# Optimization experiments

Measured on AMD Instinct MI355X. Metric: run time of the kernel, lower is better.

Reference implementation:

```python
import jax, jax.numpy as jnp
import numpy as np

WS = 2
D = 128  # hidden_dim per direction
SCALE_X = float(np.sqrt(2.0))  # rescale=True, highway_bias=0 -> sqrt(1+exp(0))


def sru_bidir(x, W, wc, b, k):
    """Bidirectional single-layer SRU (sru lib, layer_norm=False, rescale=True).
    x: (L, N, din). Returns (L, N, 2*D)."""
    L, N, _ = x.shape
    U = (x @ W).reshape(L, N, 2, D, k)  # (L,N,dir,D,k)
    vf, vr = wc.reshape(2, 2, D)  # each (dir, D)
    bf, br = b.reshape(2, 2, D)
    # time-reverse the backward direction so one scan handles both
    U = jnp.concatenate([U[:, :, :1], U[::-1, :, 1:]], axis=2)
    if k == 4:
        xprime = U[..., 3]
    else:
        xp = x.reshape(L, N, 2, D)
        xprime = jnp.concatenate([xp[:, :, :1], xp[::-1, :, 1:]], axis=2) * SCALE_X

    def step(c, inp):
        u0, u1, u2, xpt = inp  # each (N,2,D)
        f = jax.nn.sigmoid(u1 + vf * c + bf)
        c = f * c + (1.0 - f) * u0
        r = jax.nn.sigmoid(u2 + vr * c + br)
        h = r * c + (1.0 - r) * xpt
        return c, h

    c0 = jnp.zeros((N, 2, D), dtype=x.dtype)
    _, H = jax.lax.scan(step, c0, (U[..., 0], U[..., 1], U[..., 2], xprime))
    # un-reverse backward direction outputs
    H = jnp.concatenate([H[:, :, :1], H[::-1, :, 1:]], axis=2)
    return H.reshape(L, N, 2 * D)


def setup_inputs() -> dict:
    key = jax.random.key(0)
    ks = jax.random.split(key, 6)
    B, C, Himg, Wimg = 8, 3, 224, 224
    F = WS * WS * C  # 12
    inp = {
        "x": jax.random.normal(ks[0], (B, C, Himg, Wimg), jnp.float32),
        "W1": jax.random.normal(ks[1], (F, 2 * D * 4), jnp.float32) * (1.0 / np.sqrt(F)),
        "wc1": jax.random.normal(ks[2], (2 * 2 * D,), jnp.float32) * 0.1,
        "b1": jnp.zeros((2 * 2 * D,), jnp.float32),
        "W2": jax.random.normal(ks[3], (2 * D, 2 * D * 3), jnp.float32) * (1.0 / np.sqrt(2 * D)),
        "wc2": jax.random.normal(ks[4], (2 * 2 * D,), jnp.float32) * 0.1,
        "b2": jnp.zeros((2 * 2 * D,), jnp.float32),
    }
    return inp


def reference(x, W1, wc1, b1, W2, wc2, b2):
    B, C, Himg, Wimg = x.shape
    Hp, Wp = Himg // WS, Wimg // WS
    F = WS * WS * C
    # get_valid_patches: (B, Hp, Wp, C*ws*ws) with (C, wh, ww) flatten order
    p = x.reshape(B, C, Hp, WS, Wp, WS).transpose(0, 2, 4, 1, 3, 5).reshape(B, Hp, Wp, F)
    # input_array = patches.permute(2,0,3,1) -> (Hp, B, Wp, F)
    # apply_one_direction on firstVRNN: merge Hp into batch, scan over Wp
    a1 = p.transpose(1, 0, 2, 3).reshape(Hp * B, Wp, F).transpose(1, 0, 2)  # (Wp, Hp*B, F)
    h1 = sru_bidir(a1, W1, wc1, b1, k=4)  # (Wp, Hp*B, 2D)
    h1 = h1.transpose(1, 0, 2).reshape(Hp, B, Wp, 2 * D)
    # vertical_results = out.permute(2,1,0,3) -> (Wp, B, Hp, 2D)
    v = h1.transpose(2, 1, 0, 3)
    # second direction: merge Wp into batch, scan over Hp
    a2 = v.reshape(Wp * B, Hp, 2 * D).transpose(1, 0, 2)  # (Hp, Wp*B, 2D)
    h2 = sru_bidir(a2, W2, wc2, b2, k=3)  # (Hp, Wp*B, 2D)
    h2 = h2.transpose(1, 0, 2).reshape(Wp, B, Hp, 2 * D)
    # feature_map.permute(1,3,2,0) -> (B, 2D, Hp, Wp)
    return h2.transpose(1, 3, 2, 0)
```

## Files before the change

kernel.cpp:

```cpp
#include <hip/hip_runtime.h>
#include <hip/hip_bf16.h>

typedef unsigned short ushort_t;
typedef unsigned int uint_t;

typedef __bf16 bf16x8 __attribute__((ext_vector_type(8)));
typedef float f32x4 __attribute__((ext_vector_type(4)));

__device__ __forceinline__ float bf2f(ushort_t u) {
    return __uint_as_float(((uint_t)u) << 16);
}
__device__ __forceinline__ ushort_t f2bf(float f) {
    uint_t x = __float_as_uint(f);
    uint_t r = (x + 0x7FFFu + ((x >> 16) & 1u)) >> 16;
    return (ushort_t)r;
}
__device__ __forceinline__ float sigmoidf_fast(float x) {
    return 1.0f / (1.0f + __expf(-x));
}

#define PP 12544
#define PLANE 25690112ULL

__global__ __launch_bounds__(256) void permute_w2(const float* __restrict__ W2,
                                                  ushort_t* __restrict__ W2t) {
    int i = blockIdx.x * 256 + threadIdx.x;
    int np = i >> 8;
    int k  = i & 255;
    int kk  = np >> 8;
    int rem = np & 255;
    int dir = rem >> 7;
    int d   = rem & 127;
    int oc = dir * 384 + d * 3 + kk;
    W2t[np * 256 + k] = f2bf(W2[k * 768 + oc]);
}

__global__ __launch_bounds__(256) void scan1(const float* __restrict__ x,
                                             const float* __restrict__ W1,
                                             const float* __restrict__ wc1,
                                             const float* __restrict__ b1,
                                             ushort_t* __restrict__ H1a,
                                             ushort_t* __restrict__ U2t) {
    __shared__ float patch[112 * 12];
    __shared__ ushort_t hbuf[112 * 258];
    const int n1 = blockIdx.x;
    const int hp = n1 >> 3, b = n1 & 7;
    const int tid = threadIdx.x;
    const float SCALE_X = 1.41421356237309515f;

    for (int e = tid; e < 1344; e += 256) {
        int c = e / 448;
        int rem = e % 448;
        int wh = rem / 224;
        int pos = rem % 224;
        float v = x[((b * 3 + c) * 224 + (2 * hp + wh)) * 224 + pos];
        patch[(pos >> 1) * 12 + c * 4 + wh * 2 + (pos & 1)] = v;
    }

    float4 w[12];
    const float4* W1v = (const float4*)W1;
#pragma unroll
    for (int j = 0; j < 12; ++j) w[j] = W1v[j * 256 + tid];

    const float vf = wc1[tid],       vr = wc1[256 + tid];
    const float bfv = b1[tid],       brv = b1[256 + tid];
    const int dir = tid >> 7;

    __syncthreads();

    float cst = 0.0f;
    for (int t = 0; t < 112; ++t) {
        const int tt = dir ? (111 - t) : t;
        const float4* pp = (const float4*)(patch + tt * 12);
        float4 p0 = pp[0], p1 = pp[1], p2 = pp[2];
        float pj[12] = {p0.x, p0.y, p0.z, p0.w, p1.x, p1.y, p1.z, p1.w,
                        p2.x, p2.y, p2.z, p2.w};
        float u0 = 0.f, u1 = 0.f, u2 = 0.f, u3 = 0.f;
#pragma unroll
        for (int j = 0; j < 12; ++j) {
            float pv = pj[j];
            u0 = fmaf(w[j].x, pv, u0);
            u1 = fmaf(w[j].y, pv, u1);
            u2 = fmaf(w[j].z, pv, u2);
            u3 = fmaf(w[j].w, pv, u3);
        }
        float f = sigmoidf_fast(u1 + vf * cst + bfv);
        cst = f * cst + (1.0f - f) * u0;
        float r = sigmoidf_fast(u2 + vr * cst + brv);
        float h = r * cst + (1.0f - r) * u3;
        H1a[((size_t)b * PP + hp * 112 + tt) * 256 + tid] = f2bf(h);
        hbuf[tt * 258 + tid] = f2bf(h * SCALE_X);
    }

    __syncthreads();
    const size_t base3 = 3 * PLANE + (size_t)b * 256 * PP + (size_t)hp * 112;
    for (int e = tid; e < 28672; e += 256) {
        int ch = e / 112;
        int wp = e - ch * 112;
        U2t[base3 + (size_t)ch * PP + wp] = hbuf[wp * 258 + ch];
    }
}

__global__ __launch_bounds__(256) void gemm2(const ushort_t* __restrict__ A,
                                             const ushort_t* __restrict__ Bt,
                                             ushort_t* __restrict__ U2t) {
    __shared__ ushort_t As[2][128 * 32];
    __shared__ ushort_t Bs[2][128 * 32];
    const int m0 = blockIdx.y * 128;
    const int bb = blockIdx.y / 98;
    const int p0 = (blockIdx.y % 98) * 128;
    const int n0 = blockIdx.x * 128;
    const int kidx = n0 >> 8;
    const int ch0  = n0 & 255;
    const int tid = threadIdx.x;
    const int w = tid >> 6, lane = tid & 63;
    const int wm = w >> 1, wn = w & 1;
    const int lr = lane >> 2;
    const int lc = (lane & 3) * 8;
    const int ln16 = lane & 15;
    const int k8 = (lane >> 4) * 8;

    f32x4 acc[4][4] = {};

    for (int kb = 0; kb < 256; kb += 64) {
        if (kb) __syncthreads();
#pragma unroll
        for (int h = 0; h < 2; ++h) {
#pragma unroll
            for (int q = 0; q < 2; ++q) {
                int r = w * 32 + q * 16;
                const ushort_t* gA = A + (size_t)(m0 + r + lr) * 256 + kb + h * 32 + lc;
                __builtin_amdgcn_global_load_lds(
                    (const __attribute__((address_space(1))) uint_t*)gA,
                    (__attribute__((address_space(3))) uint_t*)(As[h] + r * 32), 16, 0, 0);
                const ushort_t* gB = Bt + (size_t)(n0 + r + lr) * 256 + kb + h * 32 + lc;
                __builtin_amdgcn_global_load_lds(
                    (const __attribute__((address_space(1))) uint_t*)gB,
                    (__attribute__((address_space(3))) uint_t*)(Bs[h] + r * 32), 16, 0, 0);
            }
        }
        __syncthreads();

#pragma unroll
        for (int h = 0; h < 2; ++h) {
            bf16x8 af[4], bf[4];
#pragma unroll
            for (int i = 0; i < 4; ++i) {
                af[i] = *(const bf16x8*)(As[h] + (wm * 64 + i * 16 + ln16) * 32 + k8);
                bf[i] = *(const bf16x8*)(Bs[h] + (wn * 64 + i * 16 + ln16) * 32 + k8);
            }
#pragma unroll
            for (int i = 0; i < 4; ++i)
#pragma unroll
                for (int j = 0; j < 4; ++j)
                    acc[i][j] = __builtin_amdgcn_mfma_f32_16x16x32_bf16(
                        af[i], bf[j], acc[i][j], 0, 0, 0);
        }
    }

    const int rq = (lane >> 4) * 4;
    const size_t planeBase = (size_t)kidx * PLANE + (size_t)(bb * 256 + ch0) * PP;
#pragma unroll
    for (int i = 0; i < 4; ++i) {
        int p = p0 + wm * 64 + i * 16 + rq;
#pragma unroll
        for (int j = 0; j < 4; ++j) {
            int ch_l = wn * 64 + j * 16 + ln16;
            ushort4 v;
            v.x = f2bf(acc[i][j][0]);
            v.y = f2bf(acc[i][j][1]);
            v.z = f2bf(acc[i][j][2]);
            v.w = f2bf(acc[i][j][3]);
            *(ushort4*)(U2t + planeBase + (size_t)ch_l * PP + p) = v;
        }
    }
}

__global__ __launch_bounds__(256) void scan2(const ushort_t* __restrict__ U2t,
                                             const float* __restrict__ wc2,
                                             const float* __restrict__ b2,
                                             float* __restrict__ out) {
    const int cb = blockIdx.x;
    const int b  = blockIdx.y;
    const int tid = threadIdx.x;
    const int ch = cb * 2 + (tid >> 7);
    const int wp = tid & 127;
    if (wp >= 112) return;
    const int dir = ch >> 7;

    const float vf = wc2[ch],  vr = wc2[256 + ch];
    const float bfv = b2[ch],  brv = b2[256 + ch];

    const int tt0 = dir ? 111 : 0;
    const long dstep = dir ? -112 : 112;
    const long ostep = dir ? -112 : 112;

    const ushort_t* P = U2t;
    long q    = (long)((size_t)(b * 256 + ch) * PP) + tt0 * 112 + wp;
    long oOff = (long)((size_t)(b * 256 + ch) * 112 + tt0) * 112 + wp;

    ushort_t x0 = P[q], x1 = P[PLANE + q], x2 = P[2 * PLANE + q], x3 = P[3 * PLANE + q];
    q += dstep;
    ushort_t y0 = P[q], y1 = P[PLANE + q], y2 = P[2 * PLANE + q], y3 = P[3 * PLANE + q];
    q += dstep;
    ushort_t z0 = P[q], z1 = P[PLANE + q], z2 = P[2 * PLANE + q], z3 = P[3 * PLANE + q];

    float cst = 0.0f;
    for (int t = 0; t < 112; ++t) {
        long qn = q + ((t < 109) ? dstep : 0);
        ushort_t w0 = P[qn], w1 = P[PLANE + qn], w2 = P[2 * PLANE + qn], w3 = P[3 * PLANE + qn];

        float u0 = bf2f(x0), u1 = bf2f(x1), u2v = bf2f(x2);
        float xp = bf2f(x3);
        float f = sigmoidf_fast(u1 + vf * cst + bfv);
        cst = f * cst + (1.0f - f) * u0;
        float r = sigmoidf_fast(u2v + vr * cst + brv);
        out[oOff] = r * cst + (1.0f - r) * xp;

        x0 = y0; x1 = y1; x2 = y2; x3 = y3;
        y0 = z0; y1 = z1; y2 = z2; y3 = z3;
        z0 = w0; z1 = w1; z2 = w2; z3 = w3;
        q = qn;
        oOff += ostep;
    }
}

extern "C" void kernel_launch(void* const* d_in, const int* in_sizes, int n_in,
                              void* d_out, int out_size, void* d_ws, size_t ws_size,
                              hipStream_t stream) {
    const float* x   = (const float*)d_in[0];
    const float* W1  = (const float*)d_in[1];
    const float* wc1 = (const float*)d_in[2];
    const float* b1  = (const float*)d_in[3];
    const float* W2  = (const float*)d_in[4];
    const float* wc2 = (const float*)d_in[5];
    const float* b2  = (const float*)d_in[6];
    float* out = (float*)d_out;

    char* ws = (char*)d_ws;
    ushort_t* H1a = (ushort_t*)(ws);
    ushort_t* U2t = (ushort_t*)(ws + 51380224);
    ushort_t* W2t = (ushort_t*)(ws + 51380224 + 205520896);

    permute_w2<<<768, 256, 0, stream>>>(W2, W2t);
    scan1<<<896, 256, 0, stream>>>(x, W1, wc1, b1, H1a, U2t);
    gemm2<<<dim3(6, 784), 256, 0, stream>>>(H1a, W2t, U2t);
    scan2<<<dim3(128, 8), 256, 0, stream>>>(U2t, wc2, b2, out);
}
```

Measured before the change: 381.8 us.

## Move transposed x-prime plane write from scan1 into gemm2 tile loads

scan1 no longer stages scaled h in a large shared buffer and writes the transposed fourth U2t plane. Instead, gemm2 blocks with blockIdx.x<4 write that plane from the A tiles already resident in shared memory, once per k-chunk, and scan2 applies the sqrt(2) scale. This removes scan1's ~58KB shared buffer, which should raise its occupancy, and drops a sync plus a transpose pass. The cost is some extra shared reads and global stores in part of the gemm2 blocks, and the x-prime plane now holds bf16 h that is scaled after rounding.

```diff
diff --git a/kernel.cpp b/kernel.cpp
--- a/kernel.cpp
+++ b/kernel.cpp
@@ -6,6 +6,7 @@
 
 typedef __bf16 bf16x8 __attribute__((ext_vector_type(8)));
 typedef float f32x4 __attribute__((ext_vector_type(4)));
+typedef ushort_t us8 __attribute__((ext_vector_type(8)));
 
 __device__ __forceinline__ float bf2f(ushort_t u) {
     return __uint_as_float(((uint_t)u) << 16);
@@ -39,14 +40,11 @@
                                              const float* __restrict__ W1,
                                              const float* __restrict__ wc1,
                                              const float* __restrict__ b1,
-                                             ushort_t* __restrict__ H1a,
-                                             ushort_t* __restrict__ U2t) {
+                                             ushort_t* __restrict__ H1a) {
     __shared__ float patch[112 * 12];
-    __shared__ ushort_t hbuf[112 * 258];
     const int n1 = blockIdx.x;
     const int hp = n1 >> 3, b = n1 & 7;
     const int tid = threadIdx.x;
-    const float SCALE_X = 1.41421356237309515f;
 
     for (int e = tid; e < 1344; e += 256) {
         int c = e / 448;
@@ -67,6 +65,8 @@
     const int dir = tid >> 7;
 
     __syncthreads();
+
+    const size_t h1base = ((size_t)b * PP + (size_t)hp * 112) * 256 + tid;
 
     float cst = 0.0f;
     for (int t = 0; t < 112; ++t) {
@@ -88,16 +88,7 @@
         cst = f * cst + (1.0f - f) * u0;
         float r = sigmoidf_fast(u2 + vr * cst + brv);
         float h = r * cst + (1.0f - r) * u3;
-        H1a[((size_t)b * PP + hp * 112 + tt) * 256 + tid] = f2bf(h);
-        hbuf[tt * 258 + tid] = f2bf(h * SCALE_X);
-    }
-
-    __syncthreads();
-    const size_t base3 = 3 * PLANE + (size_t)b * 256 * PP + (size_t)hp * 112;
-    for (int e = tid; e < 28672; e += 256) {
-        int ch = e / 112;
-        int wp = e - ch * 112;
-        U2t[base3 + (size_t)ch * PP + wp] = hbuf[wp * 258 + ch];
+        H1a[h1base + (size_t)tt * 256] = f2bf(h);
     }
 }
 
@@ -156,6 +147,23 @@
                     acc[i][j] = __builtin_amdgcn_mfma_f32_16x16x32_bf16(
                         af[i], bf[j], acc[i][j], 0, 0, 0);
         }
+
+        if (blockIdx.x < 4 && kb == (int)blockIdx.x * 64) {
+            const int cl = tid & 63;
+            const int pc = tid >> 6;
+            const int hh = cl >> 5;
+            const int cc = cl & 31;
+            const size_t p3 = 3 * PLANE
+                            + (size_t)(bb * 256 + kb + cl) * PP + p0 + pc * 32;
+#pragma unroll
+            for (int j8 = 0; j8 < 4; ++j8) {
+                us8 v;
+#pragma unroll
+                for (int j = 0; j < 8; ++j)
+                    v[j] = As[hh][(pc * 32 + j8 * 8 + j) * 32 + cc];
+                *(us8*)(U2t + p3 + j8 * 8) = v;
+            }
+        }
     }
 
     const int rq = (lane >> 4) * 4;
@@ -187,6 +195,7 @@
     const int wp = tid & 127;
     if (wp >= 112) return;
     const int dir = ch >> 7;
+    const float SCALE_X = 1.41421356237309515f;
 
     const float vf = wc2[ch],  vr = wc2[256 + ch];
     const float bfv = b2[ch],  brv = b2[256 + ch];
@@ -211,7 +220,7 @@
         ushort_t w0 = P[qn], w1 = P[PLANE + qn], w2 = P[2 * PLANE + qn], w3 = P[3 * PLANE + qn];
 
         float u0 = bf2f(x0), u1 = bf2f(x1), u2v = bf2f(x2);
-        float xp = bf2f(x3);
+        float xp = bf2f(x3) * SCALE_X;
         float f = sigmoidf_fast(u1 + vf * cst + bfv);
         cst = f * cst + (1.0f - f) * u0;
         float r = sigmoidf_fast(u2v + vr * cst + brv);
@@ -243,7 +252,7 @@
     ushort_t* W2t = (ushort_t*)(ws + 51380224 + 205520896);
 
     permute_w2<<<768, 256, 0, stream>>>(W2, W2t);
-    scan1<<<896, 256, 0, stream>>>(x, W1, wc1, b1, H1a, U2t);
+    scan1<<<896, 256, 0, stream>>>(x, W1, wc1, b1, H1a);
     gemm2<<<dim3(6, 784), 256, 0, stream>>>(H1a, W2t, U2t);
     scan2<<<dim3(128, 8), 256, 0, stream>>>(U2t, wc2, b2, out);
 }
```

New measurement: 382.4 us. About the same (+0.2%).
